# Kernel tuning notes

Measured on AMD Instinct MI355X. Metric: run time of the kernel, lower is better.

The kernel has to match this reference:

```python
import jax, jax.numpy as jnp
import numpy as np

N = 4096
IN_DIM = 256
OUT_DIM = 256
E = 131072


def setup_inputs() -> dict:
    key = jax.random.key(0)
    ks = jax.random.split(key, 8)
    x = jax.random.normal(ks[0], (N, IN_DIM), dtype=jnp.float32)
    edge_index = jax.random.randint(ks[1], (2, E), 0, N, dtype=jnp.int64)
    lap = jax.random.normal(ks[2], (N, N), dtype=jnp.float32)
    d_inv = jax.random.normal(ks[3], (N, N), dtype=jnp.float32)
    # parameters
    W_high = jax.random.normal(ks[4], (IN_DIM, OUT_DIM), dtype=jnp.float32) / np.sqrt(IN_DIM)
    W_conv = jax.random.normal(ks[5], (IN_DIM, OUT_DIM), dtype=jnp.float32) / np.sqrt(IN_DIM)
    b_conv = jnp.zeros((OUT_DIM,), dtype=jnp.float32)
    aL = jax.random.uniform(ks[6], (1,), dtype=jnp.float32)
    aH = jax.random.uniform(ks[7], (1,), dtype=jnp.float32)
    return {"x": x, "edge_index": edge_index, "lap": lap, "d_inv": d_inv,
            "W_high": W_high, "W_conv": W_conv, "b_conv": b_conv,
            "aL": aL, "aH": aH}


def _gcn_conv(x, edge_index, W, b, num_nodes):
    # PyG GCNConv: add self-loops, symmetric normalization, aggregate at target.
    src, dst = edge_index[0], edge_index[1]
    loop = jnp.arange(num_nodes, dtype=edge_index.dtype)
    src_f = jnp.concatenate([src, loop])
    dst_f = jnp.concatenate([dst, loop])
    deg = jax.ops.segment_sum(jnp.ones_like(dst_f, dtype=x.dtype), dst_f,
                              num_segments=num_nodes)
    deg_inv_sqrt = jnp.where(deg > 0, jax.lax.rsqrt(jnp.maximum(deg, 1e-12)), 0.0)
    norm = deg_inv_sqrt[src_f] * deg_inv_sqrt[dst_f]  # [E+N]
    xw = x @ W                                        # [N, out]
    msgs = xw[src_f] * norm[:, None]                  # [E+N, out]
    out = jax.ops.segment_sum(msgs, dst_f, num_segments=num_nodes)
    return out + b


def reference(x, edge_index, lap, d_inv, W_high, W_conv, b_conv, aL, aH):
    # high-pass branch: Lhp = d_inv @ lap @ d_inv; Hh = Lhp @ relu(x @ W_high)
    Lhp = (d_inv @ lap) @ d_inv
    Hh = Lhp @ jax.nn.relu(x @ W_high)
    # low-pass branch: GCNConv
    Hl = _gcn_conv(x, edge_index, W_conv, b_conv, x.shape[0])
    return aL * Hl + aH * Hh
```

## Files before the change

kernel.cpp:

```cpp
#include <hip/hip_runtime.h>

#define NN 4096
#define DD 256
#define EE 131072

typedef __attribute__((ext_vector_type(8))) short s16x8;
typedef __attribute__((ext_vector_type(4))) float f32x4;

__device__ __forceinline__ unsigned short f2bf(float f) {
  unsigned u = __builtin_bit_cast(unsigned, f);
  u += 0x7FFFu + ((u >> 16) & 1u);
  return (unsigned short)(u >> 16);
}

__device__ __forceinline__ ushort4 cvt4(f32x4 v) {
  ushort4 r;
  r.x = f2bf(v[0]); r.y = f2bf(v[1]); r.z = f2bf(v[2]); r.w = f2bf(v[3]);
  return r;
}

__device__ __forceinline__ unsigned cvt2_rhu(float a, float b) {
  unsigned ua = __builtin_bit_cast(unsigned, a) + 0x8000u;
  unsigned ub = __builtin_bit_cast(unsigned, b) + 0x8000u;
  return __builtin_amdgcn_perm(ub, ua, 0x07060302u);
}

__device__ __forceinline__ uint4 pack8(f32x4 a, f32x4 b) {
  uint4 r;
  r.x = cvt2_rhu(a[0], a[1]); r.y = cvt2_rhu(a[2], a[3]);
  r.z = cvt2_rhu(b[0], b[1]); r.w = cvt2_rhu(b[2], b[3]);
  return r;
}


__global__ void k_prep(const int* __restrict__ ei, int* __restrict__ deg,
                       const float* __restrict__ Wh, const float* __restrict__ Wc,
                       unsigned short* __restrict__ WFh, unsigned short* __restrict__ WFc) {
  int t = blockIdx.x * 256 + threadIdx.x;
  if (t < EE) {
    atomicAdd(&deg[ei[EE + t]], 1);
  } else {
    int idx = t - EE;
    int which = idx >> 16;
    int r = idx & 65535;
    int n = r & 255, k = r >> 8;
    const float* W = which ? Wc : Wh;
    unsigned short* WF = which ? WFc : WFh;
    long fidx = ((long)((n >> 4) * 8 + (k >> 5))) * 512 +
                (((k >> 3) & 3) * 16 + (n & 15)) * 8 + (k & 7);
    WF[fidx] = f2bf(W[k * 256 + n]);
  }
}

__global__ void k_scan(const int* __restrict__ deg, int* __restrict__ row_start,
                       float* __restrict__ dis) {
  __shared__ int part[1024];
  int t = threadIdx.x;
  int d0 = deg[4 * t + 0], d1 = deg[4 * t + 1], d2 = deg[4 * t + 2], d3 = deg[4 * t + 3];
  int s = d0 + d1 + d2 + d3;
  part[t] = s;
  __syncthreads();
  for (int off = 1; off < 1024; off <<= 1) {
    int add = (t >= off) ? part[t - off] : 0;
    __syncthreads();
    part[t] += add;
    __syncthreads();
  }
  int base = part[t] - s;
  row_start[4 * t + 0] = base;
  row_start[4 * t + 1] = base + d0;
  row_start[4 * t + 2] = base + d0 + d1;
  row_start[4 * t + 3] = base + d0 + d1 + d2;
  if (t == 1023) row_start[4096] = part[t];
  dis[4 * t + 0] = rsqrtf((float)d0 + 1.0f);
  dis[4 * t + 1] = rsqrtf((float)d1 + 1.0f);
  dis[4 * t + 2] = rsqrtf((float)d2 + 1.0f);
  dis[4 * t + 3] = rsqrtf((float)d3 + 1.0f);
}

__global__ void k_scatter(const int* __restrict__ ei, const int* __restrict__ row_start,
                          int* __restrict__ cursor, int* __restrict__ csr) {
  int e = blockIdx.x * 256 + threadIdx.x;
  if (e < EE) {
    int s = ei[e];
    int d = ei[EE + e];
    int p = atomicAdd(&cursor[d], 1);
    csr[row_start[d] + p] = s;
  }
}

__global__ __launch_bounds__(512) void k_xw(const float* __restrict__ x,
                                            const unsigned short* __restrict__ WFh,
                                            const unsigned short* __restrict__ WFc,
                                            unsigned short* __restrict__ RF,
                                            float* __restrict__ XWs,
                                            const float* __restrict__ dis) {
  __shared__ alignas(16) unsigned short Abuf[16][264];
  const int tid = threadIdx.x;
  const int w = tid >> 6, lane = tid & 63;
  const int quad = lane >> 4, l16 = lane & 15, quad8 = quad * 8;
  const int m0 = blockIdx.x * 16;

  {
    int srow = tid >> 5, scolf = (tid & 31) * 8;
    const float* ap = x + (long)(m0 + srow) * DD + scolf;
    f32x4 a0 = *(const f32x4*)ap;
    f32x4 a1 = *(const f32x4*)(ap + 4);
    *(uint4*)&Abuf[srow][scolf] = pack8(a0, a1);
  }
  __syncthreads();

  const bool hi = (w < 4);
  const int wo = hi ? w : (w - 4);
  const unsigned short* WF = hi ? WFh : WFc;
  const unsigned short* bp = WF + lane * 8;

  f32x4 acc[4] = {{0,0,0,0},{0,0,0,0},{0,0,0,0},{0,0,0,0}};
#pragma unroll
  for (int q = 0; q < 8; ++q) {
    s16x8 af = *(const s16x8*)&Abuf[l16][q * 32 + quad8];
#pragma unroll
    for (int s = 0; s < 4; ++s) {
      s16x8 bf = *(const s16x8*)(bp + ((long)((4 * wo + s) * 8 + q)) * 512);
      acc[s] = __builtin_amdgcn_mfma_f32_16x16x32_bf16(af, bf, acc[s], 0, 0, 0);
    }
  }

  if (hi) {
    const int kc = m0 >> 5;
    const int qp = ((m0 >> 4) & 1) * 2 + (quad >> 1);
    const int j0 = (quad & 1) * 4;
#pragma unroll
    for (int s = 0; s < 4; ++s) {
      int t = 4 * wo + s;
      f32x4 v = acc[s];
      f32x4 z;
      z[0] = v[0] > 0.f ? v[0] : 0.f;
      z[1] = v[1] > 0.f ? v[1] : 0.f;
      z[2] = v[2] > 0.f ? v[2] : 0.f;
      z[3] = v[3] > 0.f ? v[3] : 0.f;
      long idx = ((long)(t * 128 + kc)) * 512 + (qp * 16 + l16) * 8 + j0;
      *(ushort4*)(RF + idx) = cvt4(z);
    }
  } else {
    float dm[4];
#pragma unroll
    for (int r = 0; r < 4; ++r) dm[r] = dis[m0 + quad * 4 + r];
#pragma unroll
    for (int s = 0; s < 4; ++s) {
      int col = 64 * wo + 16 * s + l16;
#pragma unroll
      for (int r = 0; r < 4; ++r)
        XWs[(long)(m0 + quad * 4 + r) * DD + col] = dm[r] * acc[s][r];
    }
  }
}

__global__ void k_agg(const float* __restrict__ XWs, const int* __restrict__ row_start,
                      const int* __restrict__ csr, const float* __restrict__ dis,
                      float* __restrict__ Hl) {
  const int i = blockIdx.x;
  const int t = threadIdx.x;
  const int b0 = row_start[i], b1 = row_start[i + 1];
  float acc = XWs[(long)i * DD + t];
  int j = b0;
  for (; j + 8 <= b1; j += 8) {
    int s0 = csr[j], s1 = csr[j + 1], s2 = csr[j + 2], s3 = csr[j + 3];
    int s4 = csr[j + 4], s5 = csr[j + 5], s6 = csr[j + 6], s7 = csr[j + 7];
    float v0 = XWs[(long)s0 * DD + t];
    float v1 = XWs[(long)s1 * DD + t];
    float v2 = XWs[(long)s2 * DD + t];
    float v3 = XWs[(long)s3 * DD + t];
    float v4 = XWs[(long)s4 * DD + t];
    float v5 = XWs[(long)s5 * DD + t];
    float v6 = XWs[(long)s6 * DD + t];
    float v7 = XWs[(long)s7 * DD + t];
    acc += ((v0 + v1) + (v2 + v3)) + ((v4 + v5) + (v6 + v7));
  }
  for (; j < b1; ++j) acc += XWs[(long)csr[j] * DD + t];
  Hl[(long)i * DD + t] = dis[i] * acc;
}

#define MM3_STEP(sv, BCUR, BNXT, CUR, NXT)                                        \
  {                                                                               \
    const int sn = (sv) + 1;                                                      \
    f32x4 an[8];                                                                  \
    if (sn < 16) {                                                                \
      _Pragma("unroll")                                                           \
      for (int i = 0; i < 4; ++i) {                                               \
        an[i] = *(const f32x4*)(aptr0 + sn * 256 + 4 * i);                        \
        an[4 + i] = *(const f32x4*)(aptr1 + sn * 256 + 4 * i);                    \
      }                                                                           \
      _Pragma("unroll")                                                           \
      for (int c8 = 0; c8 < 8; ++c8)                                              \
        BNXT[c8] = *(const s16x8*)(bbase + ((long)(sn * 8 + c8)) * 512);          \
    }                                                                             \
    _Pragma("unroll")                                                             \
    for (int c8 = 0; c8 < 8; ++c8) {                                              \
      s16x8 a0 = *(const s16x8*)&Abuf[CUR][l16][c8 * 32 + quad8];                 \
      s16x8 a1 = *(const s16x8*)&Abuf[CUR][16 + l16][c8 * 32 + quad8];            \
      acc[0] = __builtin_amdgcn_mfma_f32_16x16x32_bf16(a0, BCUR[c8], acc[0], 0, 0, 0); \
      acc[1] = __builtin_amdgcn_mfma_f32_16x16x32_bf16(a1, BCUR[c8], acc[1], 0, 0, 0); \
    }                                                                             \
    if (sn < 16) {                                                                \
      *(uint4*)&Abuf[NXT][arow][acolf] = pack8(an[0], an[1]);                     \
      *(uint4*)&Abuf[NXT][arow][acolf + 8] = pack8(an[2], an[3]);                 \
      *(uint4*)&Abuf[NXT][arow + 16][acolf] = pack8(an[4], an[5]);                \
      *(uint4*)&Abuf[NXT][arow + 16][acolf + 8] = pack8(an[6], an[7]);            \
    }                                                                             \
    __syncthreads();                                                              \
  }

template <int EPI>
__global__ __launch_bounds__(256) void k_mm3(const float* __restrict__ A,
                                             const unsigned short* __restrict__ BF,
                                             unsigned short* __restrict__ CF,
                                             float* __restrict__ outF,
                                             const float* __restrict__ Hl,
                                             const float* __restrict__ bconv,
                                             const float* __restrict__ aLp,
                                             const float* __restrict__ aHp) {
  __shared__ alignas(16) unsigned short Abuf[2][32][264];
  const int tid = threadIdx.x;
  const int w = tid >> 6, lane = tid & 63;
  const int quad = lane >> 4, l16 = lane & 15, quad8 = quad * 8;
  const int m = blockIdx.x & 127;
  const int q = blockIdx.x >> 7;
  const int m0 = m * 32;
  const int tglob = q * 4 + w;

  const int arow = tid >> 4;
  const int acolf = (tid & 15) * 16;
  const float* aptr0 = A + (long)(m0 + arow) * NN + acolf;
  const float* aptr1 = aptr0 + (long)16 * NN;

  const unsigned short* bbase = BF + ((long)tglob * 128) * 512 + lane * 8;

  f32x4 acc[2] = {{0,0,0,0},{0,0,0,0}};
  s16x8 bbA[8], bbB[8];

  {
    f32x4 r0 = *(const f32x4*)(aptr0 + 0);
    f32x4 r1 = *(const f32x4*)(aptr0 + 4);
    f32x4 r2 = *(const f32x4*)(aptr0 + 8);
    f32x4 r3 = *(const f32x4*)(aptr0 + 12);
    f32x4 r4 = *(const f32x4*)(aptr1 + 0);
    f32x4 r5 = *(const f32x4*)(aptr1 + 4);
    f32x4 r6 = *(const f32x4*)(aptr1 + 8);
    f32x4 r7 = *(const f32x4*)(aptr1 + 12);
    *(uint4*)&Abuf[0][arow][acolf] = pack8(r0, r1);
    *(uint4*)&Abuf[0][arow][acolf + 8] = pack8(r2, r3);
    *(uint4*)&Abuf[0][arow + 16][acolf] = pack8(r4, r5);
    *(uint4*)&Abuf[0][arow + 16][acolf + 8] = pack8(r6, r7);
  }
#pragma unroll
  for (int c8 = 0; c8 < 8; ++c8) bbA[c8] = *(const s16x8*)(bbase + c8 * 512);
  __syncthreads();

  for (int ss = 0; ss < 8; ++ss) {
    MM3_STEP(2 * ss, bbA, bbB, 0, 1)
    MM3_STEP(2 * ss + 1, bbB, bbA, 1, 0)
  }

  if constexpr (EPI == 0) {
#pragma unroll
    for (int mu = 0; mu < 2; ++mu) {
      int qp = mu * 2 + (quad >> 1);
      int j0 = (quad & 1) * 4;
      long idx = ((long)(tglob * 128 + m)) * 512 + (qp * 16 + l16) * 8 + j0;
      *(ushort4*)(CF + idx) = cvt4(acc[mu]);
    }
  } else {
    __shared__ float obuf[32][68];
#pragma unroll
    for (int mu = 0; mu < 2; ++mu)
#pragma unroll
      for (int r = 0; r < 4; ++r)
        obuf[mu * 16 + quad * 4 + r][w * 16 + l16] = acc[mu][r];
    __syncthreads();
    const float aLv = aLp[0], aHv = aHp[0];
    const int orow = tid >> 3;
    const int ocol = (tid & 7) * 8;
    const int gcol = q * 64 + ocol;
#pragma unroll
    for (int j = 0; j < 2; ++j) {
      f32x4 cc = *(const f32x4*)&obuf[orow][ocol + 4 * j];
      f32x4 h = *(const f32x4*)(Hl + (long)(m0 + orow) * DD + gcol + 4 * j);
      f32x4 bc = *(const f32x4*)(bconv + gcol + 4 * j);
      f32x4 res;
      res[0] = aHv * cc[0] + aLv * (h[0] + bc[0]);
      res[1] = aHv * cc[1] + aLv * (h[1] + bc[1]);
      res[2] = aHv * cc[2] + aLv * (h[2] + bc[2]);
      res[3] = aHv * cc[3] + aLv * (h[3] + bc[3]);
      *(f32x4*)(outF + (long)(m0 + orow) * DD + gcol + 4 * j) = res;
    }
  }
}

extern "C" void kernel_launch(void* const* d_in, const int* in_sizes, int n_in,
                              void* d_out, int out_size, void* d_ws, size_t ws_size,
                              hipStream_t stream) {
  const float* x     = (const float*)d_in[0];
  const int*   ei    = (const int*)d_in[1];
  const float* lap   = (const float*)d_in[2];
  const float* dinv  = (const float*)d_in[3];
  const float* Wh    = (const float*)d_in[4];
  const float* Wc    = (const float*)d_in[5];
  const float* bconv = (const float*)d_in[6];
  const float* aL    = (const float*)d_in[7];
  const float* aH    = (const float*)d_in[8];
  float* out = (float*)d_out;
  char* ws = (char*)d_ws;

  int* deg        = (int*)(ws);
  int* cursor     = (int*)(ws + (16 << 10));
  int* row_start  = (int*)(ws + (32 << 10));
  int* csr        = (int*)(ws + (64 << 10));
  float* dis      = (float*)(ws + (576 << 10));
  unsigned short* WFh = (unsigned short*)(ws + (1l << 20));
  unsigned short* WFc = (unsigned short*)(ws + (1l << 20) + (128 << 10));
  unsigned short* RF  = (unsigned short*)(ws + (2l << 20));
  unsigned short* T1F = (unsigned short*)(ws + (4l << 20));
  unsigned short* T2F = (unsigned short*)(ws + (6l << 20));
  float* XWs = (float*)(ws + (8l << 20));
  float* Hl  = (float*)(ws + (12l << 20));

  hipMemsetAsync(ws, 0, 32 << 10, stream);

  k_prep<<<1024, 256, 0, stream>>>(ei, deg, Wh, Wc, WFh, WFc);
  k_scan<<<1, 1024, 0, stream>>>(deg, row_start, dis);
  k_scatter<<<512, 256, 0, stream>>>(ei, row_start, cursor, csr);
  k_xw<<<256, 512, 0, stream>>>(x, WFh, WFc, RF, XWs, dis);
  k_agg<<<4096, 256, 0, stream>>>(XWs, row_start, csr, dis, Hl);

  k_mm3<0><<<512, 256, 0, stream>>>(dinv, RF, T1F, nullptr, nullptr, nullptr, nullptr, nullptr);
  k_mm3<0><<<512, 256, 0, stream>>>(lap, T1F, T2F, nullptr, nullptr, nullptr, nullptr, nullptr);
  k_mm3<3><<<512, 256, 0, stream>>>(dinv, T2F, nullptr, out, Hl, bconv, aL, aH);
}
```

Before: 286.2 us.

## Restructure dense matmul: A fragments in registers, B tiles staged in LDS

```diff
diff --git a/kernel.cpp b/kernel.cpp
--- a/kernel.cpp
+++ b/kernel.cpp
@@ -25,11 +25,11 @@
   return __builtin_amdgcn_perm(ub, ua, 0x07060302u);
 }
 
-__device__ __forceinline__ uint4 pack8(f32x4 a, f32x4 b) {
-  uint4 r;
-  r.x = cvt2_rhu(a[0], a[1]); r.y = cvt2_rhu(a[2], a[3]);
-  r.z = cvt2_rhu(b[0], b[1]); r.w = cvt2_rhu(b[2], b[3]);
-  return r;
+__device__ __forceinline__ s16x8 frag_from(f32x4 a, f32x4 b) {
+  uint4 u;
+  u.x = cvt2_rhu(a[0], a[1]); u.y = cvt2_rhu(a[2], a[3]);
+  u.z = cvt2_rhu(b[0], b[1]); u.w = cvt2_rhu(b[2], b[3]);
+  return __builtin_bit_cast(s16x8, u);
 }
 
 
@@ -106,7 +106,10 @@
     const float* ap = x + (long)(m0 + srow) * DD + scolf;
     f32x4 a0 = *(const f32x4*)ap;
     f32x4 a1 = *(const f32x4*)(ap + 4);
-    *(uint4*)&Abuf[srow][scolf] = pack8(a0, a1);
+    uint4 u;
+    u.x = cvt2_rhu(a0[0], a0[1]); u.y = cvt2_rhu(a0[2], a0[3]);
+    u.z = cvt2_rhu(a1[0], a1[1]); u.w = cvt2_rhu(a1[2], a1[3]);
+    *(uint4*)&Abuf[srow][scolf] = u;
   }
   __syncthreads();
 
@@ -181,38 +184,42 @@
   Hl[(long)i * DD + t] = dis[i] * acc;
 }
 
-#define MM3_STEP(sv, BCUR, BNXT, CUR, NXT)                                        \
+#define MM4_STAGE(sv, CURP, NXTP)                                                 \
   {                                                                               \
     const int sn = (sv) + 1;                                                      \
-    f32x4 an[8];                                                                  \
+                     \
+    _Pragma("unroll")                                                             \
+    for (int j = 0; j < 8; ++j) AF[j] = frag_from(raw[2 * j], raw[2 * j + 1]);    \
+                                    \
     if (sn < 16) {                                                                \
       _Pragma("unroll")                                                           \
-      for (int i = 0; i < 4; ++i) {                                               \
-        an[i] = *(const f32x4*)(aptr0 + sn * 256 + 4 * i);                        \
-        an[4 + i] = *(const f32x4*)(aptr1 + sn * 256 + 4 * i);                    \
+      for (int i = 0; i < 8; ++i)                                                 \
+        breg[i] = *(const s16x8*)(bq + (long)gboff[i] + (long)sn * 4096);         \
+      _Pragma("unroll")                                                           \
+      for (int j = 0; j < 8; ++j) {                                               \
+        raw[2 * j] = *(const f32x4*)(aptr + sn * 256 + j * 32);                   \
+        raw[2 * j + 1] = *(const f32x4*)(aptr + sn * 256 + j * 32 + 4);           \
       }                                                                           \
+    }                                                                             \
+                                            \
+    _Pragma("unroll")                                                             \
+    for (int c = 0; c < 8; ++c) {                                                 \
       _Pragma("unroll")                                                           \
-      for (int c8 = 0; c8 < 8; ++c8)                                              \
-        BNXT[c8] = *(const s16x8*)(bbase + ((long)(sn * 8 + c8)) * 512);          \
+      for (int t = 0; t < 4; ++t) {                                               \
+        s16x8 bf = *(const s16x8*)(CURP + (t * 8 + c) * 512);                     \
+        acc[t] = __builtin_amdgcn_mfma_f32_16x16x32_bf16(AF[c], bf, acc[t], 0, 0, 0); \
+      }                                                                           \
     }                                                                             \
-    _Pragma("unroll")                                                             \
-    for (int c8 = 0; c8 < 8; ++c8) {                                              \
-      s16x8 a0 = *(const s16x8*)&Abuf[CUR][l16][c8 * 32 + quad8];                 \
-      s16x8 a1 = *(const s16x8*)&Abuf[CUR][16 + l16][c8 * 32 + quad8];            \
-      acc[0] = __builtin_amdgcn_mfma_f32_16x16x32_bf16(a0, BCUR[c8], acc[0], 0, 0, 0); \
-      acc[1] = __builtin_amdgcn_mfma_f32_16x16x32_bf16(a1, BCUR[c8], acc[1], 0, 0, 0); \
-    }                                                                             \
+                                      \
     if (sn < 16) {                                                                \
-      *(uint4*)&Abuf[NXT][arow][acolf] = pack8(an[0], an[1]);                     \
-      *(uint4*)&Abuf[NXT][arow][acolf + 8] = pack8(an[2], an[3]);                 \
-      *(uint4*)&Abuf[NXT][arow + 16][acolf] = pack8(an[4], an[5]);                \
-      *(uint4*)&Abuf[NXT][arow + 16][acolf + 8] = pack8(an[6], an[7]);            \
+      _Pragma("unroll")                                                           \
+      for (int i = 0; i < 8; ++i) *(s16x8*)(NXTP + (i * 4 + w) * 512) = breg[i];  \
     }                                                                             \
     __syncthreads();                                                              \
   }
 
 template <int EPI>
-__global__ __launch_bounds__(256) void k_mm3(const float* __restrict__ A,
+__global__ __launch_bounds__(256) void k_mm4(const float* __restrict__ A,
                                              const unsigned short* __restrict__ BF,
                                              unsigned short* __restrict__ CF,
                                              float* __restrict__ outF,
@@ -220,70 +227,69 @@
                                              const float* __restrict__ bconv,
                                              const float* __restrict__ aLp,
                                              const float* __restrict__ aHp) {
-  __shared__ alignas(16) unsigned short Abuf[2][32][264];
+  __shared__ alignas(16) unsigned short Bbuf[2][32][512];
   const int tid = threadIdx.x;
   const int w = tid >> 6, lane = tid & 63;
-  const int quad = lane >> 4, l16 = lane & 15, quad8 = quad * 8;
-  const int m = blockIdx.x & 127;
-  const int q = blockIdx.x >> 7;
-  const int m0 = m * 32;
-  const int tglob = q * 4 + w;
-
-  const int arow = tid >> 4;
-  const int acolf = (tid & 15) * 16;
-  const float* aptr0 = A + (long)(m0 + arow) * NN + acolf;
-  const float* aptr1 = aptr0 + (long)16 * NN;
-
-  const unsigned short* bbase = BF + ((long)tglob * 128) * 512 + lane * 8;
-
-  f32x4 acc[2] = {{0,0,0,0},{0,0,0,0}};
-  s16x8 bbA[8], bbB[8];
-
-  {
-    f32x4 r0 = *(const f32x4*)(aptr0 + 0);
-    f32x4 r1 = *(const f32x4*)(aptr0 + 4);
-    f32x4 r2 = *(const f32x4*)(aptr0 + 8);
-    f32x4 r3 = *(const f32x4*)(aptr0 + 12);
-    f32x4 r4 = *(const f32x4*)(aptr1 + 0);
-    f32x4 r5 = *(const f32x4*)(aptr1 + 4);
-    f32x4 r6 = *(const f32x4*)(aptr1 + 8);
-    f32x4 r7 = *(const f32x4*)(aptr1 + 12);
-    *(uint4*)&Abuf[0][arow][acolf] = pack8(r0, r1);
-    *(uint4*)&Abuf[0][arow][acolf + 8] = pack8(r2, r3);
-    *(uint4*)&Abuf[0][arow + 16][acolf] = pack8(r4, r5);
-    *(uint4*)&Abuf[0][arow + 16][acolf + 8] = pack8(r6, r7);
-  }
-#pragma unroll
-  for (int c8 = 0; c8 < 8; ++c8) bbA[c8] = *(const s16x8*)(bbase + c8 * 512);
+  const int quad = lane >> 4, l16 = lane & 15;
+  const int mblk = blockIdx.x & 63;
+  const int q = blockIdx.x >> 6;
+  const int m0 = mblk * 64;
+
+  const float* aptr = A + (long)(m0 + w * 16 + l16) * NN + quad * 8;
+
+  const unsigned short* bq = BF + (long)q * 4 * 128 * 512 + lane * 8;
+  int gboff[8];
+#pragma unroll
+  for (int i = 0; i < 8; ++i) {
+    int cf = i * 4 + w;
+    gboff[i] = ((cf >> 3) * 128 + (cf & 7)) * 512;
+  }
+  unsigned short* b0p = &Bbuf[0][0][0] + lane * 8;
+  unsigned short* b1p = &Bbuf[1][0][0] + lane * 8;
+
+  f32x4 raw[16];
+  s16x8 AF[8], breg[8];
+  f32x4 acc[4] = {{0,0,0,0},{0,0,0,0},{0,0,0,0},{0,0,0,0}};
+
+#pragma unroll
+  for (int i = 0; i < 8; ++i) breg[i] = *(const s16x8*)(bq + (long)gboff[i]);
+#pragma unroll
+  for (int j = 0; j < 8; ++j) {
+    raw[2 * j] = *(const f32x4*)(aptr + j * 32);
+    raw[2 * j + 1] = *(const f32x4*)(aptr + j * 32 + 4);
+  }
+#pragma unroll
+  for (int i = 0; i < 8; ++i) *(s16x8*)(b0p + (i * 4 + w) * 512) = breg[i];
   __syncthreads();
 
   for (int ss = 0; ss < 8; ++ss) {
-    MM3_STEP(2 * ss, bbA, bbB, 0, 1)
-    MM3_STEP(2 * ss + 1, bbB, bbA, 1, 0)
+    MM4_STAGE(2 * ss, b0p, b1p)
+    MM4_STAGE(2 * ss + 1, b1p, b0p)
   }
 
   if constexpr (EPI == 0) {
-#pragma unroll
-    for (int mu = 0; mu < 2; ++mu) {
-      int qp = mu * 2 + (quad >> 1);
-      int j0 = (quad & 1) * 4;
-      long idx = ((long)(tglob * 128 + m)) * 512 + (qp * 16 + l16) * 8 + j0;
-      *(ushort4*)(CF + idx) = cvt4(acc[mu]);
+    const int kc = 2 * mblk + (w >> 1);
+    const int kquad = (w & 1) * 2 + (quad >> 1);
+    const int j0 = (quad & 1) * 4;
+#pragma unroll
+    for (int t = 0; t < 4; ++t) {
+      long idx = ((long)((q * 4 + t) * 128 + kc)) * 512 + (kquad * 16 + l16) * 8 + j0;
+      *(ushort4*)(CF + idx) = cvt4(acc[t]);
     }
   } else {
-    __shared__ float obuf[32][68];
-#pragma unroll
-    for (int mu = 0; mu < 2; ++mu)
+    __shared__ float obuf[64][68];
+#pragma unroll
+    for (int t = 0; t < 4; ++t)
 #pragma unroll
       for (int r = 0; r < 4; ++r)
-        obuf[mu * 16 + quad * 4 + r][w * 16 + l16] = acc[mu][r];
+        obuf[w * 16 + quad * 4 + r][t * 16 + l16] = acc[t][r];
     __syncthreads();
     const float aLv = aLp[0], aHv = aHp[0];
-    const int orow = tid >> 3;
-    const int ocol = (tid & 7) * 8;
+    const int orow = tid >> 2;
+    const int ocol = (tid & 3) * 16;
     const int gcol = q * 64 + ocol;
 #pragma unroll
-    for (int j = 0; j < 2; ++j) {
+    for (int j = 0; j < 4; ++j) {
       f32x4 cc = *(const f32x4*)&obuf[orow][ocol + 4 * j];
       f32x4 h = *(const f32x4*)(Hl + (long)(m0 + orow) * DD + gcol + 4 * j);
       f32x4 bc = *(const f32x4*)(bconv + gcol + 4 * j);
@@ -333,7 +339,7 @@
   k_xw<<<256, 512, 0, stream>>>(x, WFh, WFc, RF, XWs, dis);
   k_agg<<<4096, 256, 0, stream>>>(XWs, row_start, csr, dis, Hl);
 
-  k_mm3<0><<<512, 256, 0, stream>>>(dinv, RF, T1F, nullptr, nullptr, nullptr, nullptr, nullptr);
-  k_mm3<0><<<512, 256, 0, stream>>>(lap, T1F, T2F, nullptr, nullptr, nullptr, nullptr, nullptr);
-  k_mm3<3><<<512, 256, 0, stream>>>(dinv, T2F, nullptr, out, Hl, bconv, aL, aH);
-}
+  k_mm4<0><<<256, 256, 0, stream>>>(dinv, RF, T1F, nullptr, nullptr, nullptr, nullptr, nullptr);
+  k_mm4<0><<<256, 256, 0, stream>>>(lap, T1F, T2F, nullptr, nullptr, nullptr, nullptr, nullptr);
+  k_mm4<3><<<256, 256, 0, stream>>>(dinv, T2F, nullptr, out, Hl, bconv, aL, aH);
+}
```

Result: slower. 301.4 us (+5.3%).
